# Optimization experiments

Hardware: AMD Instinct MI355X
Metric: run time of the kernel (lower is better)

Reference implementation:

```python
import jax, jax.numpy as jnp
import numpy as np

E = 1024
H = 16
D = E // H
S = 2048
B = 2

def setup_inputs() -> dict:
    key = jax.random.key(0)
    ks = jax.random.split(key, 5)
    x = jax.random.normal(ks[0], (B, S, E), dtype=jnp.float32)
    W_qkv = jax.random.normal(ks[1], (E, 3 * E), dtype=jnp.float32) / np.sqrt(E)
    b_qkv = jax.random.normal(ks[2], (3 * E,), dtype=jnp.float32) * 0.02
    W_out = jax.random.normal(ks[3], (E, E), dtype=jnp.float32) / np.sqrt(E)
    b_out = jax.random.normal(ks[4], (E,), dtype=jnp.float32) * 0.02
    return {"x": x, "W_qkv": W_qkv, "b_qkv": b_qkv, "W_out": W_out, "b_out": b_out}

def reference(x, W_qkv, b_qkv, W_out, b_out):
    b, s, e = x.shape
    qkv = x @ W_qkv + b_qkv                      # [B,S,3E]
    q, k, v = jnp.split(qkv, 3, axis=-1)
    # [B,S,E] -> [B,H,S,D]
    q = q.reshape(b, s, H, D).transpose(0, 2, 1, 3)
    k = k.reshape(b, s, H, D).transpose(0, 2, 1, 3)
    v = v.reshape(b, s, H, D).transpose(0, 2, 1, 3)
    scale = 1.0 / np.sqrt(D)
    att = jnp.einsum('bhqd,bhkd->bhqk', q, k) * scale
    causal = jnp.tril(jnp.ones((s, s), dtype=bool))
    att = jnp.where(causal[None, None], att, -jnp.inf)
    att = jax.nn.softmax(att, axis=-1)
    out = jnp.einsum('bhqk,bhkd->bhqd', att, v)  # [B,H,S,D]
    out = out.transpose(0, 2, 1, 3).reshape(b, s, e)
    return out @ W_out + b_out
```

## Files before the change

kernel.cpp:

```cpp
#include <hip/hip_runtime.h>

typedef unsigned short u16;
typedef __bf16  bf16x8 __attribute__((ext_vector_type(8)));
typedef float   f32x4  __attribute__((ext_vector_type(4)));
typedef unsigned int   u32x2 __attribute__((ext_vector_type(2)));
typedef unsigned int   u32x4 __attribute__((ext_vector_type(4)));
typedef unsigned short u16x4 __attribute__((ext_vector_type(4)));
typedef unsigned short u16x8 __attribute__((ext_vector_type(8)));

#define BB 2
#define HH 16
#define DD 64
#define SS 2048
#define EE 1024

#define QSCALE 0.1803368801111244f

static __device__ __forceinline__ u16 f2bf(float f) {
    unsigned int u = __float_as_uint(f);
    u += 0x7FFFu + ((u >> 16) & 1u);
    return (u16)(u >> 16);
}

static __device__ __forceinline__ unsigned int cvtpk(float lo, float hi) {
    unsigned int r;
    asm("v_cvt_pk_bf16_f32 %0, %1, %2" : "=v"(r) : "v"(lo), "v"(hi));
    return r;
}

union BfCast { u32x4 u; bf16x8 b; };
static __device__ __forceinline__ bf16x8 ldb8(const u16* p) {
    BfCast x; x.u = *(const u32x4*)p; return x.b;
}

static __device__ __forceinline__ void gload16(const u16* g, u16* l) {
    __builtin_amdgcn_global_load_lds(
        (const __attribute__((address_space(1))) unsigned int*)g,
        (__attribute__((address_space(3))) unsigned int*)l, 16, 0, 0);
}

#define UG (32 * 512)
static __device__ __forceinline__ int kidx(int s, int d) {
    return (((s >> 4) * 2 + (d >> 5)) * 512) + ((((d >> 3) & 3) * 16 + (s & 15)) * 8) + (d & 7);
}
static __device__ __forceinline__ int vidx(int key, int d) {
    return (((key >> 5) * 4 + (d >> 4)) * 512) + ((((key >> 3) & 3) * 16 + (d & 15)) * 8) + (key & 7);
}

__global__ __launch_bounds__(256) void prep_kernel(
    const float* __restrict__ x,    u16* __restrict__ xb,
    const float* __restrict__ Wqkv, u16* __restrict__ wqkvT,
    const float* __restrict__ Wout, u16* __restrict__ woutT)
{
    __shared__ float tile[32][33];
    const int bid = blockIdx.x;
    if (bid < 2048) {
        const int t = bid * 256 + threadIdx.x;
        const int u = t >> 6, w = t & 63;
        const int m = (u >> 5) * 16 + (w & 15);
        const int k = (u & 31) * 32 + (w >> 4) * 8;
        const float* p = x + m * 1024 + k;
        const f32x4 a = *(const f32x4*)p;
        const f32x4 b = *(const f32x4*)(p + 4);
        u16x8 o;
        o[0] = f2bf(a[0]); o[1] = f2bf(a[1]); o[2] = f2bf(a[2]); o[3] = f2bf(a[3]);
        o[4] = f2bf(b[0]); o[5] = f2bf(b[1]); o[6] = f2bf(b[2]); o[7] = f2bf(b[3]);
        *(u16x8*)&xb[u * 512 + w * 8] = o;
        return;
    }
    const float* in; u16* out; int C, tb;
    if (bid < 2048 + 3072) { in = Wqkv; out = wqkvT; C = 3072; tb = bid - 2048; }
    else                   { in = Wout; out = woutT; C = 1024; tb = bid - 5120; }
    const int tx = threadIdx.x & 31;
    const int ty = threadIdx.x >> 5;
    const int ct = C >> 5;
    const int bc = tb % ct, br = tb / ct;
    const int c0 = bc * 32, r0 = br * 32;
    #pragma unroll
    for (int i = 0; i < 4; i++)
        tile[ty + i * 8][tx] = in[(r0 + ty + i * 8) * C + c0 + tx];
    __syncthreads();
    #pragma unroll
    for (int i = 0; i < 4; i++) {
        const int n = c0 + ty + i * 8;
        out[((n >> 4) * 32 + (r0 >> 5)) * 512 + (((tx >> 3) & 3) * 16 + (n & 15)) * 8 + (tx & 7)]
            = f2bf(tile[tx][ty + i * 8]);
    }
}

__global__ __launch_bounds__(256) void gemm_qkv_kernel(
    const u16* __restrict__ Af,
    const u16* __restrict__ Bf,
    const float* __restrict__ bias,
    u16* __restrict__ Qb, u16* __restrict__ Kb, u16* __restrict__ Vb)
{
    __shared__ __align__(16) u16 Us[2][16 * 512];
    const int lane = threadIdx.x & 63;
    const int wave = threadIdx.x >> 6;
    const int nb = 3 * EE / 128;
    const int tm = blockIdx.x / nb, tn = blockIdx.x % nb;
    const int lm = lane & 15, quad = lane >> 4;

    const u16* sp[4];
    #pragma unroll
    for (int j = 0; j < 4; j++) {
        const int idx = 4 * wave + j;
        sp[j] = (idx < 8) ? (Af + (tm * 8 + idx) * UG + lane * 8)
                          : (Bf + (tn * 8 + idx - 8) * UG + lane * 8);
    }
    u16* ld0 = &Us[0][4 * wave * 512];
    u16* ld1 = &Us[1][4 * wave * 512];

    const int wy = wave >> 1, wx = wave & 1;
    f32x4 acc[4][4] = {};

    #pragma unroll
    for (int j = 0; j < 4; j++) gload16(sp[j], ld0 + j * 512);

    for (int it = 0; it < 32; ++it) {
        const int cur = it & 1;
        __syncthreads();
        if (it + 1 < 32) {
            u16* ld = cur ? ld0 : ld1;
            const int ko = (it + 1) * 512;
            #pragma unroll
            for (int j = 0; j < 4; j++) gload16(sp[j] + ko, ld + j * 512);
        }
        bf16x8 af[4], bf[4];
        #pragma unroll
        for (int i = 0; i < 4; i++) {
            af[i] = ldb8(&Us[cur][(wy * 4 + i) * 512 + lane * 8]);
            bf[i] = ldb8(&Us[cur][(8 + wx * 4 + i) * 512 + lane * 8]);
        }
        #pragma unroll
        for (int mi = 0; mi < 4; mi++)
            #pragma unroll
            for (int ni = 0; ni < 4; ni++)
                acc[mi][ni] = __builtin_amdgcn_mfma_f32_16x16x32_bf16(af[mi], bf[ni], acc[mi][ni], 0, 0, 0);
    }

    const int gm0 = tm * 128 + wy * 64;
    const int gn0 = tn * 128 + wx * 64;
    #pragma unroll
    for (int ni = 0; ni < 4; ni++) {
        const int n = gn0 + ni * 16 + lm;
        const float bv = bias[n];
        const int which = n >> 10;
        const int e = n & 1023;
        const int h = e >> 6, d = e & 63;
        #pragma unroll
        for (int mi = 0; mi < 4; mi++) {
            if (which == 2) {
                const int m0 = gm0 + mi * 16 + quad * 4;
                const int b = m0 >> 11, key0 = m0 & 2047;
                u16x4 pk;
                #pragma unroll
                for (int r = 0; r < 4; r++) pk[r] = f2bf(acc[mi][ni][r] + bv);
                *(u16x4*)&Vb[(b * HH + h) * 131072 + vidx(key0, d)] = pk;
            } else if (which == 1) {
                #pragma unroll
                for (int r = 0; r < 4; r++) {
                    const int m = gm0 + mi * 16 + quad * 4 + r;
                    const int b = m >> 11, s = m & 2047;
                    Kb[(b * HH + h) * 131072 + kidx(s, d)] = f2bf(acc[mi][ni][r] + bv);
                }
            } else {
                #pragma unroll
                for (int r = 0; r < 4; r++) {
                    const int m = gm0 + mi * 16 + quad * 4 + r;
                    const int b = m >> 11, s = m & 2047;
                    Qb[((b * HH + h) * SS + s) * DD + d] = f2bf((acc[mi][ni][r] + bv) * QSCALE);
                }
            }
        }
    }
}

__global__ __launch_bounds__(512) void attn_kernel(
    const u16* __restrict__ Qb, const u16* __restrict__ Kb,
    const u16* __restrict__ Vb, u16* __restrict__ Ob)
{
    __shared__ __align__(16) u16 Ks[2][4096];
    __shared__ __align__(16) u16 Vs[2][4096];
    __shared__ __align__(16) u16 Plds[8 * 16 * 72];
    const int tid = threadIdx.x;
    const int lane = tid & 63, wave = tid >> 6;
    const int lm = lane & 15, quad = lane >> 4;
    const int bh = blockIdx.x & 31;
    const int pr = blockIdx.x >> 5;
    const int qtA = 31 - pr, qtB = pr;
    const int qt_w = (wave < 4) ? qtA : qtB;
    const int qrow = qt_w * 64 + (wave & 3) * 16;
    const int b = bh >> 4, h = bh & 15;

    const u16* qbase = Qb + (bh * SS + qrow) * DD;
    const bf16x8 qf0 = ldb8(qbase + lm * DD + quad * 8);
    const bf16x8 qf1 = ldb8(qbase + lm * DD + 32 + quad * 8);

    const u16* ktile = Kb + bh * 131072;
    const u16* vtile = Vb + bh * 131072;
    u16* Pw = Plds + wave * (16 * 72);

    BfCast oc; oc.u = (u32x4){0x3F803F80u, 0x3F803F80u, 0x3F803F80u, 0x3F803F80u};
    const bf16x8 ones = oc.b;

    f32x4 oacc[4] = {};
    f32x4 lacc = {0.f, 0.f, 0.f, 0.f};

    const int ktmax = qtA + 1;
    {
        gload16(ktile + wave * 512 + lane * 8, &Ks[0][wave * 512]);
        gload16(vtile + wave * 512 + lane * 8, &Vs[0][wave * 512]);
    }
    for (int kt = 0; kt < ktmax; ++kt) {
        const int cur = kt & 1;
        const int k0 = kt * 64;
        __syncthreads();
        if (kt + 1 < ktmax) {
            gload16(ktile + (kt + 1) * 4096 + wave * 512 + lane * 8, &Ks[cur ^ 1][wave * 512]);
            gload16(vtile + (kt + 1) * 4096 + wave * 512 + lane * 8, &Vs[cur ^ 1][wave * 512]);
        }

        if (kt <= qt_w) {
            f32x4 s[4];
            #pragma unroll
            for (int g = 0; g < 4; g++) {
                f32x4 z = {0.f, 0.f, 0.f, 0.f};
                z    = __builtin_amdgcn_mfma_f32_16x16x32_bf16(ldb8(&Ks[cur][(g * 2) * 512 + lane * 8]), qf0, z, 0, 0, 0);
                s[g] = __builtin_amdgcn_mfma_f32_16x16x32_bf16(ldb8(&Ks[cur][(g * 2 + 1) * 512 + lane * 8]), qf1, z, 0, 0, 0);
            }
            if (k0 + 63 > qrow) {
                const int lim = qrow + lm - k0 - quad * 4;
                #pragma unroll
                for (int g = 0; g < 4; g++)
                    #pragma unroll
                    for (int r = 0; r < 4; r++)
                        if (g * 16 + r > lim) s[g][r] = -INFINITY;
            }
            #pragma unroll
            for (int g = 0; g < 4; g++) {
                u32x2 w;
                w[0] = cvtpk(__builtin_amdgcn_exp2f(s[g][0]), __builtin_amdgcn_exp2f(s[g][1]));
                w[1] = cvtpk(__builtin_amdgcn_exp2f(s[g][2]), __builtin_amdgcn_exp2f(s[g][3]));
                *(u32x2*)&Pw[lm * 72 + g * 16 + quad * 4] = w;
            }
            const bf16x8 pf0 = ldb8(&Pw[lm * 72 + quad * 8]);
            const bf16x8 pf1 = ldb8(&Pw[lm * 72 + 32 + quad * 8]);
            lacc = __builtin_amdgcn_mfma_f32_16x16x32_bf16(ones, pf0, lacc, 0, 0, 0);
            lacc = __builtin_amdgcn_mfma_f32_16x16x32_bf16(ones, pf1, lacc, 0, 0, 0);
            #pragma unroll
            for (int dg = 0; dg < 4; dg++) {
                oacc[dg] = __builtin_amdgcn_mfma_f32_16x16x32_bf16(ldb8(&Vs[cur][dg * 512 + lane * 8]), pf0, oacc[dg], 0, 0, 0);
                oacc[dg] = __builtin_amdgcn_mfma_f32_16x16x32_bf16(ldb8(&Vs[cur][(4 + dg) * 512 + lane * 8]), pf1, oacc[dg], 0, 0, 0);
            }
        }
    }
    const float inv = 1.0f / lacc[0];
    u16* ob = Ob + (((b * SS + qrow) >> 4) * 32 + h * 2) * 512;
    #pragma unroll
    for (int dg = 0; dg < 4; dg++) {
        u32x2 w;
        w[0] = cvtpk(oacc[dg][0] * inv, oacc[dg][1] * inv);
        w[1] = cvtpk(oacc[dg][2] * inv, oacc[dg][3] * inv);
        *(u32x2*)&ob[(dg >> 1) * 512 + (((dg * 2 + (quad >> 1)) & 3) * 16 + lm) * 8 + (quad & 1) * 4] = w;
    }
}

__global__ __launch_bounds__(256) void gemm_out_kernel(
    const u16* __restrict__ Af,
    const u16* __restrict__ Bf,
    const float* __restrict__ bias,
    float* __restrict__ Out)
{
    __shared__ __align__(16) u16 Us[2][16 * 512];
    const int lane = threadIdx.x & 63;
    const int wave = threadIdx.x >> 6;
    const int nb = EE / 128;
    const int tm = blockIdx.x / nb, tn = blockIdx.x % nb;
    const int lm = lane & 15, quad = lane >> 4;

    const u16* sp[4];
    #pragma unroll
    for (int j = 0; j < 4; j++) {
        const int idx = 4 * wave + j;
        sp[j] = (idx < 8) ? (Af + (tm * 8 + idx) * UG + lane * 8)
                          : (Bf + (tn * 8 + idx - 8) * UG + lane * 8);
    }
    u16* ld0 = &Us[0][4 * wave * 512];
    u16* ld1 = &Us[1][4 * wave * 512];

    const int wy = wave >> 1, wx = wave & 1;
    f32x4 acc[4][4] = {};

    #pragma unroll
    for (int j = 0; j < 4; j++) gload16(sp[j], ld0 + j * 512);

    for (int it = 0; it < 32; ++it) {
        const int cur = it & 1;
        __syncthreads();
        if (it + 1 < 32) {
            u16* ld = cur ? ld0 : ld1;
            const int ko = (it + 1) * 512;
            #pragma unroll
            for (int j = 0; j < 4; j++) gload16(sp[j] + ko, ld + j * 512);
        }
        bf16x8 af[4], bf[4];
        #pragma unroll
        for (int i = 0; i < 4; i++) {
            af[i] = ldb8(&Us[cur][(wy * 4 + i) * 512 + lane * 8]);
            bf[i] = ldb8(&Us[cur][(8 + wx * 4 + i) * 512 + lane * 8]);
        }
        #pragma unroll
        for (int mi = 0; mi < 4; mi++)
            #pragma unroll
            for (int ni = 0; ni < 4; ni++)
                acc[mi][ni] = __builtin_amdgcn_mfma_f32_16x16x32_bf16(af[mi], bf[ni], acc[mi][ni], 0, 0, 0);
    }

    const int gm0 = tm * 128 + wy * 64;
    const int gn0 = tn * 128 + wx * 64;
    #pragma unroll
    for (int ni = 0; ni < 4; ni++) {
        const int n = gn0 + ni * 16 + lm;
        const float bv = bias[n];
        #pragma unroll
        for (int mi = 0; mi < 4; mi++)
            #pragma unroll
            for (int r = 0; r < 4; r++)
                Out[(gm0 + mi * 16 + quad * 4 + r) * EE + n] = acc[mi][ni][r] + bv;
    }
}

extern "C" void kernel_launch(void* const* d_in, const int* in_sizes, int n_in,
                              void* d_out, int out_size, void* d_ws, size_t ws_size,
                              hipStream_t stream)
{
    const float* x     = (const float*)d_in[0];
    const float* Wqkv  = (const float*)d_in[1];
    const float* bqkv  = (const float*)d_in[2];
    const float* Wout  = (const float*)d_in[3];
    const float* bout  = (const float*)d_in[4];
    float* out = (float*)d_out;

    char* ws = (char*)d_ws;
    u16* xb    = (u16*)(ws + 0);
    u16* wqkvT = (u16*)(ws + 8388608);
    u16* woutT = (u16*)(ws + 14680064);
    u16* Qb    = (u16*)(ws + 16777216);
    u16* Kb    = (u16*)(ws + 25165824);
    u16* Vb    = (u16*)(ws + 33554432);
    u16* Ob    = (u16*)(ws + 41943040);
    if (ws_size < 50331648) return;

    prep_kernel<<<2048 + 3072 + 1024, 256, 0, stream>>>(x, xb, Wqkv, wqkvT, Wout, woutT);
    gemm_qkv_kernel<<<(BB * SS / 128) * (3 * EE / 128), 256, 0, stream>>>(xb, wqkvT, bqkv, Qb, Kb, Vb);
    attn_kernel<<<BB * HH * (SS / 128), 512, 0, stream>>>(Qb, Kb, Vb, Ob);
    gemm_out_kernel<<<(BB * SS / 128) * (EE / 128), 256, 0, stream>>>(Ob, woutT, bout, out);
}
```

Baseline: 171.8 us.

## Load K/V fragments directly from global memory, drop LDS staging and pairing

The attention kernel no longer stages K and V tiles through double-buffered shared memory with block-wide barriers. Each wave loads its K and V MFMA fragments straight from global memory into registers. Blocks now hold 4 waves on a single query tile instead of a balanced pair of tiles, launched in descending causal-work order. MFMA sections are wrapped in s_setprio to favour matrix issue. This removes the LDS traffic and __syncthreads, but multiplies global/L2 reads of K/V per wave and drops the explicit load-balancing pairing.

```diff
diff --git a/kernel.cpp b/kernel.cpp
--- a/kernel.cpp
+++ b/kernel.cpp
@@ -176,29 +176,25 @@
     }
 }
 
-__global__ __launch_bounds__(512) void attn_kernel(
+__global__ __launch_bounds__(256) void attn_kernel(
     const u16* __restrict__ Qb, const u16* __restrict__ Kb,
     const u16* __restrict__ Vb, u16* __restrict__ Ob)
 {
-    __shared__ __align__(16) u16 Ks[2][4096];
-    __shared__ __align__(16) u16 Vs[2][4096];
-    __shared__ __align__(16) u16 Plds[8 * 16 * 72];
+    __shared__ __align__(16) u16 Plds[4 * 16 * 72];
     const int tid = threadIdx.x;
     const int lane = tid & 63, wave = tid >> 6;
     const int lm = lane & 15, quad = lane >> 4;
-    const int bh = blockIdx.x & 31;
-    const int pr = blockIdx.x >> 5;
-    const int qtA = 31 - pr, qtB = pr;
-    const int qt_w = (wave < 4) ? qtA : qtB;
-    const int qrow = qt_w * 64 + (wave & 3) * 16;
+    const int bh = blockIdx.x >> 5;
+    const int qt = 31 - (blockIdx.x & 31);
+    const int qrow = qt * 64 + wave * 16;
     const int b = bh >> 4, h = bh & 15;
 
     const u16* qbase = Qb + (bh * SS + qrow) * DD;
     const bf16x8 qf0 = ldb8(qbase + lm * DD + quad * 8);
     const bf16x8 qf1 = ldb8(qbase + lm * DD + 32 + quad * 8);
 
-    const u16* ktile = Kb + bh * 131072;
-    const u16* vtile = Vb + bh * 131072;
+    const u16* ktile = Kb + bh * 131072 + lane * 8;
+    const u16* vtile = Vb + bh * 131072 + lane * 8;
     u16* Pw = Plds + wave * (16 * 72);
 
     BfCast oc; oc.u = (u32x4){0x3F803F80u, 0x3F803F80u, 0x3F803F80u, 0x3F803F80u};
@@ -207,53 +203,55 @@
     f32x4 oacc[4] = {};
     f32x4 lacc = {0.f, 0.f, 0.f, 0.f};
 
-    const int ktmax = qtA + 1;
-    {
-        gload16(ktile + wave * 512 + lane * 8, &Ks[0][wave * 512]);
-        gload16(vtile + wave * 512 + lane * 8, &Vs[0][wave * 512]);
-    }
-    for (int kt = 0; kt < ktmax; ++kt) {
-        const int cur = kt & 1;
+    for (int kt = 0; kt <= qt; ++kt) {
         const int k0 = kt * 64;
-        __syncthreads();
-        if (kt + 1 < ktmax) {
-            gload16(ktile + (kt + 1) * 4096 + wave * 512 + lane * 8, &Ks[cur ^ 1][wave * 512]);
-            gload16(vtile + (kt + 1) * 4096 + wave * 512 + lane * 8, &Vs[cur ^ 1][wave * 512]);
-        }
-
-        if (kt <= qt_w) {
-            f32x4 s[4];
-            #pragma unroll
-            for (int g = 0; g < 4; g++) {
-                f32x4 z = {0.f, 0.f, 0.f, 0.f};
-                z    = __builtin_amdgcn_mfma_f32_16x16x32_bf16(ldb8(&Ks[cur][(g * 2) * 512 + lane * 8]), qf0, z, 0, 0, 0);
-                s[g] = __builtin_amdgcn_mfma_f32_16x16x32_bf16(ldb8(&Ks[cur][(g * 2 + 1) * 512 + lane * 8]), qf1, z, 0, 0, 0);
-            }
-            if (k0 + 63 > qrow) {
-                const int lim = qrow + lm - k0 - quad * 4;
+        const u16* kp = ktile + kt * 4096;
+        const u16* vp = vtile + kt * 4096;
+
+        bf16x8 kf[8];
+        #pragma unroll
+        for (int u = 0; u < 8; u++) kf[u] = ldb8(kp + u * 512);
+
+        f32x4 s[4];
+        __builtin_amdgcn_s_setprio(1);
+        #pragma unroll
+        for (int g = 0; g < 4; g++) {
+            f32x4 z = {0.f, 0.f, 0.f, 0.f};
+            z    = __builtin_amdgcn_mfma_f32_16x16x32_bf16(kf[g * 2],     qf0, z, 0, 0, 0);
+            s[g] = __builtin_amdgcn_mfma_f32_16x16x32_bf16(kf[g * 2 + 1], qf1, z, 0, 0, 0);
+        }
+        __builtin_amdgcn_s_setprio(0);
+
+        bf16x8 vf[8];
+        #pragma unroll
+        for (int u = 0; u < 8; u++) vf[u] = ldb8(vp + u * 512);
+
+        if (k0 + 63 > qrow) {
+            const int lim = qrow + lm - k0 - quad * 4;
+            #pragma unroll
+            for (int g = 0; g < 4; g++)
                 #pragma unroll
-                for (int g = 0; g < 4; g++)
-                    #pragma unroll
-                    for (int r = 0; r < 4; r++)
-                        if (g * 16 + r > lim) s[g][r] = -INFINITY;
-            }
-            #pragma unroll
-            for (int g = 0; g < 4; g++) {
-                u32x2 w;
-                w[0] = cvtpk(__builtin_amdgcn_exp2f(s[g][0]), __builtin_amdgcn_exp2f(s[g][1]));
-                w[1] = cvtpk(__builtin_amdgcn_exp2f(s[g][2]), __builtin_amdgcn_exp2f(s[g][3]));
-                *(u32x2*)&Pw[lm * 72 + g * 16 + quad * 4] = w;
-            }
-            const bf16x8 pf0 = ldb8(&Pw[lm * 72 + quad * 8]);
-            const bf16x8 pf1 = ldb8(&Pw[lm * 72 + 32 + quad * 8]);
-            lacc = __builtin_amdgcn_mfma_f32_16x16x32_bf16(ones, pf0, lacc, 0, 0, 0);
-            lacc = __builtin_amdgcn_mfma_f32_16x16x32_bf16(ones, pf1, lacc, 0, 0, 0);
-            #pragma unroll
-            for (int dg = 0; dg < 4; dg++) {
-                oacc[dg] = __builtin_amdgcn_mfma_f32_16x16x32_bf16(ldb8(&Vs[cur][dg * 512 + lane * 8]), pf0, oacc[dg], 0, 0, 0);
-                oacc[dg] = __builtin_amdgcn_mfma_f32_16x16x32_bf16(ldb8(&Vs[cur][(4 + dg) * 512 + lane * 8]), pf1, oacc[dg], 0, 0, 0);
-            }
-        }
+                for (int r = 0; r < 4; r++)
+                    if (g * 16 + r > lim) s[g][r] = -INFINITY;
+        }
+        #pragma unroll
+        for (int g = 0; g < 4; g++) {
+            u32x2 w;
+            w[0] = cvtpk(__builtin_amdgcn_exp2f(s[g][0]), __builtin_amdgcn_exp2f(s[g][1]));
+            w[1] = cvtpk(__builtin_amdgcn_exp2f(s[g][2]), __builtin_amdgcn_exp2f(s[g][3]));
+            *(u32x2*)&Pw[lm * 72 + g * 16 + quad * 4] = w;
+        }
+        const bf16x8 pf0 = ldb8(&Pw[lm * 72 + quad * 8]);
+        const bf16x8 pf1 = ldb8(&Pw[lm * 72 + 32 + quad * 8]);
+        __builtin_amdgcn_s_setprio(1);
+        lacc = __builtin_amdgcn_mfma_f32_16x16x32_bf16(ones, pf0, lacc, 0, 0, 0);
+        lacc = __builtin_amdgcn_mfma_f32_16x16x32_bf16(ones, pf1, lacc, 0, 0, 0);
+        #pragma unroll
+        for (int dg = 0; dg < 4; dg++) {
+            oacc[dg] = __builtin_amdgcn_mfma_f32_16x16x32_bf16(vf[dg],     pf0, oacc[dg], 0, 0, 0);
+            oacc[dg] = __builtin_amdgcn_mfma_f32_16x16x32_bf16(vf[4 + dg], pf1, oacc[dg], 0, 0, 0);
+        }
+        __builtin_amdgcn_s_setprio(0);
     }
     const float inv = 1.0f / lacc[0];
     u16* ob = Ob + (((b * SS + qrow) >> 4) * 32 + h * 2) * 512;
@@ -354,6 +352,6 @@
 
     prep_kernel<<<2048 + 3072 + 1024, 256, 0, stream>>>(x, xb, Wqkv, wqkvT, Wout, woutT);
     gemm_qkv_kernel<<<(BB * SS / 128) * (3 * EE / 128), 256, 0, stream>>>(xb, wqkvT, bqkv, Qb, Kb, Vb);
-    attn_kernel<<<BB * HH * (SS / 128), 512, 0, stream>>>(Qb, Kb, Vb, Ob);
+    attn_kernel<<<BB * HH * (SS / 64), 256, 0, stream>>>(Qb, Kb, Vb, Ob);
     gemm_out_kernel<<<(BB * SS / 128) * (EE / 128), 256, 0, stream>>>(Ob, woutT, bout, out);
 }
```

New measurement: 198.3 us. 15.5% more time.

## Software-pipeline attention loop: overlap PV of previous tile with QK of current

Applied to the files above, without the earlier changes.

Restructures the attention inner loop so each iteration issues the QK^T MFMAs for the current key tile together with the P·V MFMAs for the previous tile's probabilities. V is triple-buffered and P is double-buffered in LDS so the previous tile's data stays valid one extra iteration, and an epilogue drains the last tile. This is meant to hide the exp/convert/LDS round-trip latency behind independent matrix work, at the cost of more LDS and more complex buffer indexing.

```diff
diff --git a/kernel.cpp b/kernel.cpp
--- a/kernel.cpp
+++ b/kernel.cpp
@@ -181,8 +181,8 @@
     const u16* __restrict__ Vb, u16* __restrict__ Ob)
 {
     __shared__ __align__(16) u16 Ks[2][4096];
-    __shared__ __align__(16) u16 Vs[2][4096];
-    __shared__ __align__(16) u16 Plds[8 * 16 * 72];
+    __shared__ __align__(16) u16 Vs[3][4096];
+    __shared__ __align__(16) u16 Plds[2][8 * 16 * 72];
     const int tid = threadIdx.x;
     const int lane = tid & 63, wave = tid >> 6;
     const int lm = lane & 15, quad = lane >> 4;
@@ -199,7 +199,7 @@
 
     const u16* ktile = Kb + bh * 131072;
     const u16* vtile = Vb + bh * 131072;
-    u16* Pw = Plds + wave * (16 * 72);
+    const int pw = wave * 1152;
 
     BfCast oc; oc.u = (u32x4){0x3F803F80u, 0x3F803F80u, 0x3F803F80u, 0x3F803F80u};
     const bf16x8 ones = oc.b;
@@ -213,21 +213,36 @@
         gload16(vtile + wave * 512 + lane * 8, &Vs[0][wave * 512]);
     }
     for (int kt = 0; kt < ktmax; ++kt) {
-        const int cur = kt & 1;
         const int k0 = kt * 64;
         __syncthreads();
         if (kt + 1 < ktmax) {
-            gload16(ktile + (kt + 1) * 4096 + wave * 512 + lane * 8, &Ks[cur ^ 1][wave * 512]);
-            gload16(vtile + (kt + 1) * 4096 + wave * 512 + lane * 8, &Vs[cur ^ 1][wave * 512]);
-        }
+            gload16(ktile + (kt + 1) * 4096 + wave * 512 + lane * 8, &Ks[(kt + 1) & 1][wave * 512]);
+            gload16(vtile + (kt + 1) * 4096 + wave * 512 + lane * 8, &Vs[(kt + 1) % 3][wave * 512]);
+        }
+        const int rb = (kt & 1) ^ 1;
+        const int vb3 = (kt + 2) % 3;
 
         if (kt <= qt_w) {
+            bf16x8 pf0, pf1;
+            if (kt > 0) {
+                pf0 = ldb8(&Plds[rb][pw + lm * 72 + quad * 8]);
+                pf1 = ldb8(&Plds[rb][pw + lm * 72 + 32 + quad * 8]);
+            }
             f32x4 s[4];
             #pragma unroll
             for (int g = 0; g < 4; g++) {
                 f32x4 z = {0.f, 0.f, 0.f, 0.f};
-                z    = __builtin_amdgcn_mfma_f32_16x16x32_bf16(ldb8(&Ks[cur][(g * 2) * 512 + lane * 8]), qf0, z, 0, 0, 0);
-                s[g] = __builtin_amdgcn_mfma_f32_16x16x32_bf16(ldb8(&Ks[cur][(g * 2 + 1) * 512 + lane * 8]), qf1, z, 0, 0, 0);
+                z    = __builtin_amdgcn_mfma_f32_16x16x32_bf16(ldb8(&Ks[kt & 1][(g * 2) * 512 + lane * 8]), qf0, z, 0, 0, 0);
+                s[g] = __builtin_amdgcn_mfma_f32_16x16x32_bf16(ldb8(&Ks[kt & 1][(g * 2 + 1) * 512 + lane * 8]), qf1, z, 0, 0, 0);
+            }
+            if (kt > 0) {
+                lacc = __builtin_amdgcn_mfma_f32_16x16x32_bf16(ones, pf0, lacc, 0, 0, 0);
+                lacc = __builtin_amdgcn_mfma_f32_16x16x32_bf16(ones, pf1, lacc, 0, 0, 0);
+                #pragma unroll
+                for (int dg = 0; dg < 4; dg++) {
+                    oacc[dg] = __builtin_amdgcn_mfma_f32_16x16x32_bf16(ldb8(&Vs[vb3][dg * 512 + lane * 8]),       pf0, oacc[dg], 0, 0, 0);
+                    oacc[dg] = __builtin_amdgcn_mfma_f32_16x16x32_bf16(ldb8(&Vs[vb3][(4 + dg) * 512 + lane * 8]), pf1, oacc[dg], 0, 0, 0);
+                }
             }
             if (k0 + 63 > qrow) {
                 const int lim = qrow + lm - k0 - quad * 4;
@@ -242,17 +257,31 @@
                 u32x2 w;
                 w[0] = cvtpk(__builtin_amdgcn_exp2f(s[g][0]), __builtin_amdgcn_exp2f(s[g][1]));
                 w[1] = cvtpk(__builtin_amdgcn_exp2f(s[g][2]), __builtin_amdgcn_exp2f(s[g][3]));
-                *(u32x2*)&Pw[lm * 72 + g * 16 + quad * 4] = w;
-            }
-            const bf16x8 pf0 = ldb8(&Pw[lm * 72 + quad * 8]);
-            const bf16x8 pf1 = ldb8(&Pw[lm * 72 + 32 + quad * 8]);
+                *(u32x2*)&Plds[kt & 1][pw + lm * 72 + g * 16 + quad * 4] = w;
+            }
+        } else if (kt == qt_w + 1) {
+            const bf16x8 pf0 = ldb8(&Plds[rb][pw + lm * 72 + quad * 8]);
+            const bf16x8 pf1 = ldb8(&Plds[rb][pw + lm * 72 + 32 + quad * 8]);
             lacc = __builtin_amdgcn_mfma_f32_16x16x32_bf16(ones, pf0, lacc, 0, 0, 0);
             lacc = __builtin_amdgcn_mfma_f32_16x16x32_bf16(ones, pf1, lacc, 0, 0, 0);
             #pragma unroll
             for (int dg = 0; dg < 4; dg++) {
-                oacc[dg] = __builtin_amdgcn_mfma_f32_16x16x32_bf16(ldb8(&Vs[cur][dg * 512 + lane * 8]), pf0, oacc[dg], 0, 0, 0);
-                oacc[dg] = __builtin_amdgcn_mfma_f32_16x16x32_bf16(ldb8(&Vs[cur][(4 + dg) * 512 + lane * 8]), pf1, oacc[dg], 0, 0, 0);
-            }
+                oacc[dg] = __builtin_amdgcn_mfma_f32_16x16x32_bf16(ldb8(&Vs[vb3][dg * 512 + lane * 8]),       pf0, oacc[dg], 0, 0, 0);
+                oacc[dg] = __builtin_amdgcn_mfma_f32_16x16x32_bf16(ldb8(&Vs[vb3][(4 + dg) * 512 + lane * 8]), pf1, oacc[dg], 0, 0, 0);
+            }
+        }
+    }
+    if (wave < 4) {
+        const int rb = qtA & 1;
+        const int vb3 = qtA % 3;
+        const bf16x8 pf0 = ldb8(&Plds[rb][pw + lm * 72 + quad * 8]);
+        const bf16x8 pf1 = ldb8(&Plds[rb][pw + lm * 72 + 32 + quad * 8]);
+        lacc = __builtin_amdgcn_mfma_f32_16x16x32_bf16(ones, pf0, lacc, 0, 0, 0);
+        lacc = __builtin_amdgcn_mfma_f32_16x16x32_bf16(ones, pf1, lacc, 0, 0, 0);
+        #pragma unroll
+        for (int dg = 0; dg < 4; dg++) {
+            oacc[dg] = __builtin_amdgcn_mfma_f32_16x16x32_bf16(ldb8(&Vs[vb3][dg * 512 + lane * 8]),       pf0, oacc[dg], 0, 0, 0);
+            oacc[dg] = __builtin_amdgcn_mfma_f32_16x16x32_bf16(ldb8(&Vs[vb3][(4 + dg) * 512 + lane * 8]), pf1, oacc[dg], 0, 0, 0);
         }
     }
     const float inv = 1.0f / lacc[0];
```

After: 165.0 us. -4.0%, faster.
